# Optimization experiments

Measured on AMD Instinct MI355X. Metric: run time of the kernel, lower is better.

Reference implementation:

```python
import jax, jax.numpy as jnp
import numpy as np

N_NODES = 100000
N_EDGES = 1600000
D_FEAT = 128
NUM_LAYERS = 2
LN_EPS = 1e-5


def setup_inputs() -> dict:
    key = jax.random.key(0)
    k1, k2 = jax.random.split(key)
    x = jax.random.normal(k1, (N_NODES, D_FEAT), dtype=jnp.float32)
    edge_index = jax.random.randint(k2, (2, N_EDGES), 0, N_NODES, dtype=jnp.int64)
    return {"x": x, "edge_index": edge_index}


def _layernorm(h):
    # LayerNorm(elementwise_affine=False): normalize over last dim, no scale/shift
    mu = jnp.mean(h, axis=-1, keepdims=True)
    var = jnp.mean(jnp.square(h - mu), axis=-1, keepdims=True)
    return (h - mu) * jax.lax.rsqrt(var + LN_EPS)


def reference(x, edge_index):
    dst = edge_index[0]  # output rows of adj_t (out[i] = sum_j A[i,j] x[j])
    src = edge_index[1]  # gathered source nodes
    n = x.shape[0]

    # norm = rsqrt(1 + row_degree); adjacency is fixed so compute once
    deg = jax.ops.segment_sum(jnp.ones(src.shape[0], x.dtype), dst, num_segments=n)
    norm = jax.lax.rsqrt(1.0 + deg)[:, None]  # [N, 1]

    def conv(h):
        h = norm * h
        agg = jax.ops.segment_sum(h[src], dst, num_segments=n) + h  # SpMM + self residual
        return norm * agg

    ori = x
    for i in range(NUM_LAYERS):
        if i != 0:
            x = x + ori            # residual
            x = _layernorm(x)      # affine-free LayerNorm (dropout=0)
        x = conv(x)
    return x + ori
```

## Files before the change

kernel.cpp:

```cpp
#include <hip/hip_runtime.h>

#define D_FEAT 128
#define TILE 2048
#define RB 256
#define CAPE 4864

typedef float floatx2 __attribute__((ext_vector_type(2)));
typedef int int8v __attribute__((ext_vector_type(8)));

__device__ __forceinline__ unsigned int f32pair_to_bf16x2(float a, float b) {
    unsigned int ua = __float_as_uint(a);
    ua += 0x7fffu + ((ua >> 16) & 1u);
    unsigned int ub = __float_as_uint(b);
    ub += 0x7fffu + ((ub >> 16) & 1u);
    return (ua >> 16) | (ub & 0xffff0000u);
}

__global__ __launch_bounds__(512) void bin_sort(const int* __restrict__ ei, int E,
                                                int* __restrict__ gcursor,
                                                unsigned int* __restrict__ packed,
                                                int NB2) {
    __shared__ int h[512], lstart[512], cur[512], base_g[512], wsum[8];
    __shared__ unsigned int sorted[TILE];
    __shared__ unsigned short sbin[TILE];
    int t = threadIdx.x;
    h[t] = 0;
    __syncthreads();
    int tile = blockIdx.x * TILE;
    int cnt = min(TILE, E - tile);
    for (int k = t; k < cnt; k += 512)
        atomicAdd(&h[ei[tile + k] >> 8], 1);
    __syncthreads();
    if (t < NB2)
        base_g[t] = t * CAPE + (h[t] ? atomicAdd(&gcursor[t], h[t]) : 0);
    {
        int lane = t & 63;
        int w = t >> 6;
        int v = h[t];
        int incl = v;
        #pragma unroll
        for (int o = 1; o < 64; o <<= 1) {
            int nv = __shfl_up(incl, o, 64);
            if (lane >= o) incl += nv;
        }
        if (lane == 63) wsum[w] = incl;
        __syncthreads();
        int offw = 0;
        for (int w2 = 0; w2 < w; ++w2) offw += wsum[w2];
        int excl = offw + incl - v;
        lstart[t] = excl;
        cur[t] = excl;
    }
    __syncthreads();
    for (int k = t; k < cnt; k += 512) {
        int e = tile + k;
        int d = ei[e];
        int s = ei[E + e];
        int b = d >> 8;
        int r = atomicAdd(&cur[b], 1);
        sorted[r] = ((unsigned int)(d & (RB - 1)) << 17) | (unsigned int)s;
        sbin[r] = (unsigned short)b;
    }
    __syncthreads();
    for (int k = t; k < cnt; k += 512) {
        int b = sbin[k];
        packed[(long)base_g[b] + (k - lstart[b])] = sorted[k];
    }
}

__global__ __launch_bounds__(512) void build2(const unsigned int* __restrict__ packed,
                                              const int* __restrict__ gcursor,
                                              int* __restrict__ rowstart,
                                              int* __restrict__ rowcnt,
                                              float* __restrict__ norm,
                                              int* __restrict__ esrc, int N) {
    __shared__ int h[256], cur[256], wsum[4];
    int b = blockIdx.x;
    int t = threadIdx.x;
    long base = (long)b * CAPE;
    int cnt = min(gcursor[b], CAPE);
    if (t < 256) h[t] = 0;
    __syncthreads();
    for (int k = t; k < cnt; k += 512)
        atomicAdd(&h[packed[base + k] >> 17], 1);
    __syncthreads();
    if (t < 256) {
        int lane = t & 63;
        int w = t >> 6;
        int v = h[t];
        int incl = v;
        #pragma unroll
        for (int o = 1; o < 64; o <<= 1) {
            int nv = __shfl_up(incl, o, 64);
            if (lane >= o) incl += nv;
        }
        if (lane == 63) wsum[w] = incl;
        __syncthreads();
        int off = 0;
        for (int w2 = 0; w2 < w; ++w2) off += wsum[w2];
        int excl = off + incl - v;
        int row = b * RB + t;
        if (row < N) {
            rowstart[row] = (int)(base + excl);
            rowcnt[row] = v;
            norm[row] = rsqrtf(1.0f + (float)v);
        }
        cur[t] = excl;
    } else {
        __syncthreads();
    }
    __syncthreads();
    for (int k = t; k < cnt; k += 512) {
        unsigned int p = packed[base + k];
        int r = atomicAdd(&cur[p >> 17], 1);
        esrc[base + r] = (int)(p & 0x1ffffu);
    }
}

__global__ __launch_bounds__(256) void cvt2(const float* __restrict__ x,
                                            const float* __restrict__ norm,
                                            unsigned int* __restrict__ xq4,
                                            unsigned int* __restrict__ hq4,
                                            uint2* __restrict__ xb4, int N) {
    int i = blockIdx.x * 256 + threadIdx.x;
    int total = (N + 1) * 32;
    if (i >= total) return;
    int row = i >> 5;
    if (row == N) {
        xq4[i] = 0;
        hq4[i] = 0;
        return;
    }
    float4 v = ((const float4*)x)[i];
    uint2 bb;
    bb.x = f32pair_to_bf16x2(v.x, v.y);
    bb.y = f32pair_to_bf16x2(v.z, v.w);
    xb4[i] = bb;
    float nr = norm[row];
    int q = __builtin_amdgcn_cvt_pk_fp8_f32(nr * v.x, nr * v.y, 0, false);
    q = __builtin_amdgcn_cvt_pk_fp8_f32(nr * v.z, nr * v.w, q, true);
    xq4[i] = (unsigned int)q;
}

template <int LAYER>
__global__ __launch_bounds__(256) void conv8(const unsigned short* __restrict__ xq,
                                             unsigned short* __restrict__ hq,
                                             const unsigned int* __restrict__ xb,
                                             float* __restrict__ out,
                                             const float* __restrict__ norm,
                                             const int* __restrict__ rowstart,
                                             const int* __restrict__ rowcnt,
                                             const int* __restrict__ esrc,
                                             int N) {
    int lane = threadIdx.x & 63;
    int row = blockIdx.x * 4 + (threadIdx.x >> 6);
    if (row >= N) return;
    int r0 = __builtin_amdgcn_readfirstlane(rowstart[row]);
    int cnt = __builtin_amdgcn_readfirstlane(rowcnt[row]);
    const unsigned short* gq = (LAYER == 0) ? xq : hq;
    const int* ep = esrc + r0;

    floatx2 acc = {0.f, 0.f};
    for (int qb = 0; qb < cnt; qb += 16) {
        int8v ja, jb;
        asm volatile("s_load_dwordx8 %0, %2, 0x0\n\t"
                     "s_load_dwordx8 %1, %2, 0x20\n\t"
                     "s_waitcnt lgkmcnt(0)"
                     : "=s"(ja), "=s"(jb)
                     : "s"(ep + qb));
        unsigned int hv[16];
        #pragma unroll
        for (int u = 0; u < 16; ++u) {
            int j = (u < 8) ? ja[u] : jb[u - 8];
            j = (qb + u < cnt) ? j : N;
            hv[u] = gq[j * 64 + lane];
        }
        #pragma unroll
        for (int u = 0; u < 16; ++u)
            acc += __builtin_amdgcn_cvt_pk_f32_fp8((int)hv[u], false);
    }

    float ni = norm[row];
    long idx = (long)row * 64 + lane;
    unsigned int xv2 = xb[idx];
    float x0 = __uint_as_float(xv2 << 16);
    float x1 = __uint_as_float(xv2 & 0xffff0000u);

    if (LAYER == 0) {
        float o0 = ni * (acc.x + ni * x0) + x0;
        float o1 = ni * (acc.y + ni * x1) + x1;
        float s = o0 + o1;
        #pragma unroll
        for (int m = 1; m < 64; m <<= 1) s += __shfl_xor(s, m);
        float mean = s * (1.0f / 128.0f);
        o0 -= mean; o1 -= mean;
        float vs = o0 * o0 + o1 * o1;
        #pragma unroll
        for (int m = 1; m < 64; m <<= 1) vs += __shfl_xor(vs, m);
        float rstd = rsqrtf(vs * (1.0f / 128.0f) + 1e-5f) * ni;
        int p = __builtin_amdgcn_cvt_pk_fp8_f32(o0 * rstd, o1 * rstd, 0, false);
        hq[idx] = (unsigned short)(p & 0xffff);
    } else {
        floatx2 sv = __builtin_amdgcn_cvt_pk_f32_fp8((int)gq[idx], false);
        float o0 = ni * (acc.x + sv.x) + x0;
        float o1 = ni * (acc.y + sv.y) + x1;
        ((float2*)out)[idx] = make_float2(o0, o1);
    }
}


extern "C" void kernel_launch(void* const* d_in, const int* in_sizes, int n_in,
                              void* d_out, int out_size, void* d_ws, size_t ws_size,
                              hipStream_t stream) {
    const float* x = (const float*)d_in[0];
    const int* ei = (const int*)d_in[1];
    int N = in_sizes[0] / D_FEAT;
    int E = in_sizes[1] / 2;
    float* out = (float*)d_out;
    int NB2 = (N + RB - 1) / RB;

    char* ws = (char*)d_ws;
    size_t off = 0;
    auto alloc = [&](size_t bytes) -> void* {
        size_t cur = (off + 511) & ~(size_t)511;
        off = cur + bytes;
        return (void*)(ws + cur);
    };
    int* gcursor         = (int*)alloc(512 * 4);
    unsigned int* packed = (unsigned int*)alloc((size_t)NB2 * CAPE * 4);
    int* rowstart        = (int*)alloc((size_t)N * 4);
    int* rowcnt          = (int*)alloc((size_t)N * 4);
    int* esrc            = (int*)alloc((size_t)NB2 * CAPE * 4);
    float* norm          = (float*)alloc((size_t)N * 4);
    unsigned short* xq   = (unsigned short*)alloc((size_t)(N + 1) * 64 * 2);
    unsigned short* hq   = (unsigned short*)alloc((size_t)(N + 1) * 64 * 2);
    unsigned int* xb     = (unsigned int*)alloc((size_t)N * 64 * 4);
    (void)ws_size; (void)n_in; (void)out_size;

    (void)hipMemsetAsync(gcursor, 0, 512 * 4, stream);

    int tb = (E + TILE - 1) / TILE;
    bin_sort<<<tb, 512, 0, stream>>>(ei, E, gcursor, packed, NB2);
    build2<<<NB2, 512, 0, stream>>>(packed, gcursor, rowstart, rowcnt, norm, esrc, N);
    int cvb = ((N + 1) * 32 + 255) / 256;
    cvt2<<<cvb, 256, 0, stream>>>(x, norm, (unsigned int*)xq, (unsigned int*)hq,
                                  (uint2*)xb, N);

    conv8<0><<<(N + 3) / 4, 256, 0, stream>>>(xq, hq, xb, nullptr, norm, rowstart, rowcnt, esrc, N);
    conv8<1><<<(N + 3) / 4, 256, 0, stream>>>(xq, hq, xb, out, norm, rowstart, rowcnt, esrc, N);
}
```

Baseline: 143.5 us.

## Split layer-1 hidden features into four column slabs for cache-local gathers

Layer 0 now writes its fp8 output in four 32-byte column slabs, each holding every node's slice, instead of one 128-byte row per node. The layer-1 aggregation launches four times as many blocks, each reading one slab. Four groups of 16 lanes gather different neighbors in parallel and are combined with cross-lane shuffles. The goal is a smaller gather working set per pass so it stays in cache and more neighbors are in flight. The cost is reloading edge indices four times, smaller memory transactions, and only a quarter of lanes doing the epilogue.

```diff
diff --git a/kernel.cpp b/kernel.cpp
--- a/kernel.cpp
+++ b/kernel.cpp
@@ -120,15 +120,16 @@
 __global__ __launch_bounds__(256) void cvt2(const float* __restrict__ x,
                                             const float* __restrict__ norm,
                                             unsigned int* __restrict__ xq4,
-                                            unsigned int* __restrict__ hq4,
+                                            unsigned int* __restrict__ hqsm4,
                                             uint2* __restrict__ xb4, int N) {
     int i = blockIdx.x * 256 + threadIdx.x;
     int total = (N + 1) * 32;
     if (i >= total) return;
     int row = i >> 5;
+    int c = i & 31;
     if (row == N) {
         xq4[i] = 0;
-        hq4[i] = 0;
+        hqsm4[(size_t)(c >> 3) * (N + 1) * 8 + (size_t)N * 8 + (c & 7)] = 0;
         return;
     }
     float4 v = ((const float4*)x)[i];
@@ -142,22 +143,19 @@
     xq4[i] = (unsigned int)q;
 }
 
-template <int LAYER>
-__global__ __launch_bounds__(256) void conv8(const unsigned short* __restrict__ xq,
-                                             unsigned short* __restrict__ hq,
-                                             const unsigned int* __restrict__ xb,
-                                             float* __restrict__ out,
-                                             const float* __restrict__ norm,
-                                             const int* __restrict__ rowstart,
-                                             const int* __restrict__ rowcnt,
-                                             const int* __restrict__ esrc,
-                                             int N) {
+__global__ __launch_bounds__(256) void conv_l0(const unsigned short* __restrict__ xq,
+                                               unsigned short* __restrict__ hq_sm,
+                                               const unsigned int* __restrict__ xb,
+                                               const float* __restrict__ norm,
+                                               const int* __restrict__ rowstart,
+                                               const int* __restrict__ rowcnt,
+                                               const int* __restrict__ esrc,
+                                               int N) {
     int lane = threadIdx.x & 63;
     int row = blockIdx.x * 4 + (threadIdx.x >> 6);
     if (row >= N) return;
     int r0 = __builtin_amdgcn_readfirstlane(rowstart[row]);
     int cnt = __builtin_amdgcn_readfirstlane(rowcnt[row]);
-    const unsigned short* gq = (LAYER == 0) ? xq : hq;
     const int* ep = esrc + r0;
 
     floatx2 acc = {0.f, 0.f};
@@ -173,7 +171,7 @@
         for (int u = 0; u < 16; ++u) {
             int j = (u < 8) ? ja[u] : jb[u - 8];
             j = (qb + u < cnt) ? j : N;
-            hv[u] = gq[j * 64 + lane];
+            hv[u] = xq[j * 64 + lane];
         }
         #pragma unroll
         for (int u = 0; u < 16; ++u)
@@ -186,25 +184,73 @@
     float x0 = __uint_as_float(xv2 << 16);
     float x1 = __uint_as_float(xv2 & 0xffff0000u);
 
-    if (LAYER == 0) {
-        float o0 = ni * (acc.x + ni * x0) + x0;
-        float o1 = ni * (acc.y + ni * x1) + x1;
-        float s = o0 + o1;
-        #pragma unroll
-        for (int m = 1; m < 64; m <<= 1) s += __shfl_xor(s, m);
-        float mean = s * (1.0f / 128.0f);
-        o0 -= mean; o1 -= mean;
-        float vs = o0 * o0 + o1 * o1;
-        #pragma unroll
-        for (int m = 1; m < 64; m <<= 1) vs += __shfl_xor(vs, m);
-        float rstd = rsqrtf(vs * (1.0f / 128.0f) + 1e-5f) * ni;
-        int p = __builtin_amdgcn_cvt_pk_fp8_f32(o0 * rstd, o1 * rstd, 0, false);
-        hq[idx] = (unsigned short)(p & 0xffff);
-    } else {
-        floatx2 sv = __builtin_amdgcn_cvt_pk_f32_fp8((int)gq[idx], false);
+    float o0 = ni * (acc.x + ni * x0) + x0;
+    float o1 = ni * (acc.y + ni * x1) + x1;
+    float s = o0 + o1;
+    #pragma unroll
+    for (int m = 1; m < 64; m <<= 1) s += __shfl_xor(s, m);
+    float mean = s * (1.0f / 128.0f);
+    o0 -= mean; o1 -= mean;
+    float vs = o0 * o0 + o1 * o1;
+    #pragma unroll
+    for (int m = 1; m < 64; m <<= 1) vs += __shfl_xor(vs, m);
+    float rstd = rsqrtf(vs * (1.0f / 128.0f) + 1e-5f) * ni;
+    int p = __builtin_amdgcn_cvt_pk_fp8_f32(o0 * rstd, o1 * rstd, 0, false);
+    hq_sm[(size_t)(lane >> 4) * (N + 1) * 16 + (size_t)row * 16 + (lane & 15)] =
+        (unsigned short)(p & 0xffff);
+}
+
+__global__ __launch_bounds__(256) void conv1_sl(const unsigned short* __restrict__ hq_sm,
+                                                const unsigned int* __restrict__ xb,
+                                                float* __restrict__ out,
+                                                const float* __restrict__ norm,
+                                                const int* __restrict__ rowstart,
+                                                const int* __restrict__ rowcnt,
+                                                const int* __restrict__ esrc,
+                                                int N) {
+    int lane = threadIdx.x & 63;
+    int w = threadIdx.x >> 6;
+    int s = blockIdx.x & 3;
+    int row = (blockIdx.x >> 2) * 4 + w;
+    if (row >= N) return;
+    int nb = lane >> 4;
+    int col = lane & 15;
+    int r0 = __builtin_amdgcn_readfirstlane(rowstart[row]);
+    int cnt = __builtin_amdgcn_readfirstlane(rowcnt[row]);
+    const unsigned short* hs = hq_sm + (size_t)s * (N + 1) * 16;
+
+    floatx2 acc = {0.f, 0.f};
+    for (int qb = 0; qb < cnt; qb += 16) {
+        int jv[4];
+        #pragma unroll
+        for (int q = 0; q < 4; ++q)
+            jv[q] = esrc[r0 + qb + 4 * q + nb];
+        unsigned short hv[4];
+        #pragma unroll
+        for (int q = 0; q < 4; ++q) {
+            unsigned int ju = min((unsigned int)jv[q], (unsigned int)N);
+            ju = (qb + 4 * q + nb < cnt) ? ju : (unsigned int)N;
+            hv[q] = hs[ju * 16 + col];
+        }
+        #pragma unroll
+        for (int q = 0; q < 4; ++q)
+            acc += __builtin_amdgcn_cvt_pk_f32_fp8((int)hv[q], false);
+    }
+    acc.x += __shfl_xor(acc.x, 16);
+    acc.y += __shfl_xor(acc.y, 16);
+    acc.x += __shfl_xor(acc.x, 32);
+    acc.y += __shfl_xor(acc.y, 32);
+
+    if (nb == 0) {
+        float ni = norm[row];
+        floatx2 sv = __builtin_amdgcn_cvt_pk_f32_fp8((int)hs[(size_t)row * 16 + col], false);
+        long fidx = (long)row * 64 + s * 16 + col;
+        unsigned int xv2 = xb[fidx];
+        float x0 = __uint_as_float(xv2 << 16);
+        float x1 = __uint_as_float(xv2 & 0xffff0000u);
         float o0 = ni * (acc.x + sv.x) + x0;
         float o1 = ni * (acc.y + sv.y) + x1;
-        ((float2*)out)[idx] = make_float2(o0, o1);
+        ((float2*)out)[fidx] = make_float2(o0, o1);
     }
 }
 
@@ -230,10 +276,10 @@
     unsigned int* packed = (unsigned int*)alloc((size_t)NB2 * CAPE * 4);
     int* rowstart        = (int*)alloc((size_t)N * 4);
     int* rowcnt          = (int*)alloc((size_t)N * 4);
-    int* esrc            = (int*)alloc((size_t)NB2 * CAPE * 4);
+    int* esrc            = (int*)alloc((size_t)NB2 * CAPE * 4 + 256);
     float* norm          = (float*)alloc((size_t)N * 4);
     unsigned short* xq   = (unsigned short*)alloc((size_t)(N + 1) * 64 * 2);
-    unsigned short* hq   = (unsigned short*)alloc((size_t)(N + 1) * 64 * 2);
+    unsigned short* hqsm = (unsigned short*)alloc((size_t)4 * (N + 1) * 16 * 2);
     unsigned int* xb     = (unsigned int*)alloc((size_t)N * 64 * 4);
     (void)ws_size; (void)n_in; (void)out_size;
 
@@ -243,9 +289,10 @@
     bin_sort<<<tb, 512, 0, stream>>>(ei, E, gcursor, packed, NB2);
     build2<<<NB2, 512, 0, stream>>>(packed, gcursor, rowstart, rowcnt, norm, esrc, N);
     int cvb = ((N + 1) * 32 + 255) / 256;
-    cvt2<<<cvb, 256, 0, stream>>>(x, norm, (unsigned int*)xq, (unsigned int*)hq,
+    cvt2<<<cvb, 256, 0, stream>>>(x, norm, (unsigned int*)xq, (unsigned int*)hqsm,
                                   (uint2*)xb, N);
 
-    conv8<0><<<(N + 3) / 4, 256, 0, stream>>>(xq, hq, xb, nullptr, norm, rowstart, rowcnt, esrc, N);
-    conv8<1><<<(N + 3) / 4, 256, 0, stream>>>(xq, hq, xb, out, norm, rowstart, rowcnt, esrc, N);
-}
+    conv_l0<<<(N + 3) / 4, 256, 0, stream>>>(xq, hqsm, xb, norm, rowstart, rowcnt, esrc, N);
+    int g1 = ((N + 3) / 4) * 4;
+    conv1_sl<<<g1, 256, 0, stream>>>(hqsm, xb, out, norm, rowstart, rowcnt, esrc, N);
+}
```

After: 216.5 us. 1.51x slower.
